# Kernel tuning notes

Measured on AMD Instinct MI355X. Metric: run time of the kernel, lower is better.

The kernel has to match this reference:

```python
import jax, jax.numpy as jnp
import numpy as np

N_NODES = 100000
N_EDGES = 1600000
VOCAB = 128
D = 30
N_CLASSES = 5


def setup_inputs() -> dict:
    key = jax.random.key(0)
    ks = jax.random.split(key, 8)
    x = jax.random.randint(ks[0], (N_NODES,), 0, VOCAB)
    edge_index = jax.random.randint(ks[1], (2, N_EDGES), 0, N_NODES)
    emb = jax.random.normal(ks[2], (VOCAB, D), dtype=jnp.float32)
    W1 = jax.random.normal(ks[3], (D, D), dtype=jnp.float32) * (1.0 / np.sqrt(D))
    W2 = jax.random.normal(ks[4], (D, D), dtype=jnp.float32) * (1.0 / np.sqrt(D))
    W3 = jax.random.normal(ks[5], (D, D), dtype=jnp.float32) * (1.0 / np.sqrt(D))
    Wout = jax.random.normal(ks[6], (N_CLASSES, D), dtype=jnp.float32) * (1.0 / np.sqrt(D))
    b1 = jnp.zeros((D,), jnp.float32)
    b2 = jnp.zeros((D,), jnp.float32)
    b3 = jnp.zeros((D,), jnp.float32)
    bout = jnp.zeros((N_CLASSES,), jnp.float32)
    return dict(x=x, edge_index=edge_index, emb=emb, W1=W1, b1=b1, W2=W2, b2=b2,
                W3=W3, b3=b3, Wout=Wout, bout=bout)


def _gnn_layer(h, row, col, W, b):
    # h: [N, D]; row/col: [E+N] (self loops appended)
    n = h.shape[0]
    deg = jax.ops.segment_sum(jnp.ones(row.shape, h.dtype), row, num_segments=n)  # [N]
    msg = h[row] / deg[row][:, None]                 # gather + normalize: [E+N, D]
    agg = jax.ops.segment_sum(msg, col, num_segments=n)  # scatter-add: [N, D]
    return jax.nn.relu(agg @ W.T + b)


def reference(x, edge_index, emb, W1, b1, W2, b2, W3, b3, Wout, bout):
    n = x.shape[0]
    loops = jnp.arange(n, dtype=edge_index.dtype)
    row = jnp.concatenate([edge_index[0], loops])  # add_self_loops
    col = jnp.concatenate([edge_index[1], loops])
    h = emb[x]  # [N, D]
    for W, b in ((W1, b1), (W2, b2), (W3, b3)):
        h = _gnn_layer(h, row, col, W, b)
    return h @ Wout.T + bout  # [N, 5]
```

## Files before the change

kernel.cpp:

```cpp
#include <hip/hip_runtime.h>
#include <hip/hip_fp16.h>

#define D 30
#define DP 32
#define NCLS 5
#define VOCAB 128
#define BS 256
#define BSS 512
#define BSHIFT 8
#define BNODES 256
#define NSBMAX 512
#define CAP 8192
#define NBLK_S 256
#define CHUNK 6272
#define LDSCAP 8192
#define NPB 64


__global__ void k_prep(int* __restrict__ gcur, int* __restrict__ rcur, int nsb,
                       const float* __restrict__ emb, float* __restrict__ embp,
                       __half* __restrict__ A0, __half* __restrict__ A1,
                       int2* __restrict__ xr, int n) {
    int i = blockIdx.x * blockDim.x + threadIdx.x;
    if (i < nsb) { gcur[i] = i * CAP; rcur[i] = i * CAP; }
    if (i < VOCAB * DP) {
        int v = i >> 5, c = i & (DP - 1);
        embp[i] = (c < D) ? emb[v * D + c] : 0.0f;
    }
    if (i < DP) {
        A0[(size_t)n * DP + i] = __float2half_rn(0.0f);
        A1[(size_t)n * DP + i] = __float2half_rn(0.0f);
    }
    if (i == 0) xr[n] = make_int2(0, 0);
}

__global__ void __launch_bounds__(BSS)
k_scatter3(const int* __restrict__ row, const int* __restrict__ col,
           int* __restrict__ gcur, int* __restrict__ rcur,
           int* __restrict__ ebuf, unsigned char* __restrict__ rbuf,
           int e, int nsb) {
    __shared__ int pay[CHUNK];
    __shared__ unsigned short bof[CHUNK];
    __shared__ int lhist[NSBMAX];
    __shared__ int lscan[NSBMAX];
    __shared__ int lcur[NSBMAX];
    __shared__ int gdst[NSBMAX];
    unsigned char* pay8 = (unsigned char*)pay;

    int phase = blockIdx.x >= NBLK_S;
    int blk = blockIdx.x - phase * NBLK_S;
    const int* key = phase ? row : col;
    int per = (e + NBLK_S - 1) / NBLK_S;
    int s = blk * per; if (s > e) s = e;
    int t = s + per; if (t > e) t = e;
    int m = t - s;
    int tid = threadIdx.x;

    lhist[tid] = 0;
    __syncthreads();
    for (int i = s + tid; i < t; i += BSS)
        atomicAdd(&lhist[key[i] >> BSHIFT], 1);
    __syncthreads();
    lscan[tid] = lhist[tid];
    __syncthreads();
    for (int st = 1; st < NSBMAX; st <<= 1) {
        int tv = (tid >= st) ? lscan[tid - st] : 0;
        __syncthreads();
        lscan[tid] += tv;
        __syncthreads();
    }
    lcur[tid] = lscan[tid] - lhist[tid];
    __syncthreads();
    if (phase == 0) {
        for (int i = s + tid; i < t; i += BSS) {
            int c = col[i], b = c >> BSHIFT;
            int p = atomicAdd(&lcur[b], 1);
            pay[p] = (row[i] << BSHIFT) | (c & (BNODES - 1));
            bof[p] = (unsigned short)b;
        }
    } else {
        for (int i = s + tid; i < t; i += BSS) {
            int r = row[i], b = r >> BSHIFT;
            int p = atomicAdd(&lcur[b], 1);
            pay8[p] = (unsigned char)(r & (BNODES - 1));
            bof[p] = (unsigned short)b;
        }
    }
    __syncthreads();
    int* cur = phase ? rcur : gcur;
    if (tid < nsb) {
        int h = lhist[tid];
        gdst[tid] = h ? atomicAdd(&cur[tid], h) : 0;
    }
    __syncthreads();
    if (phase == 0) {
        for (int p = tid; p < m; p += BSS) {
            int b = bof[p];
            ebuf[gdst[b] + (p - (lscan[b] - lhist[b]))] = pay[p];
        }
    } else {
        for (int p = tid; p < m; p += BSS) {
            int b = bof[p];
            rbuf[gdst[b] + (p - (lscan[b] - lhist[b]))] = pay8[p];
        }
    }
}

__global__ void __launch_bounds__(BS)
k_odbsort(int* __restrict__ ebuf, const unsigned char* __restrict__ rbuf,
          const int* __restrict__ gcur, const int* __restrict__ rcur,
          const int* __restrict__ x, float* __restrict__ rdeg, int2* __restrict__ xr,
          int* __restrict__ off, int* __restrict__ cnt, int n, int nsb) {
    __shared__ int ledge[LDSCAP];
    __shared__ int c256[BNODES];
    __shared__ int p256[BNODES];
    __shared__ int b256[BNODES];
    __shared__ int cur256[BNODES];
    int side = blockIdx.x >= nsb;
    int bkt = side ? blockIdx.x - nsb : blockIdx.x;
    int tid = threadIdx.x;
    int base = bkt * CAP;

    if (side == 0) {
        int rm = rcur[bkt] - base;
        c256[tid] = 0;
        __syncthreads();
        for (int k = tid; k < rm; k += BS)
            atomicAdd(&c256[rbuf[base + k]], 1);
        __syncthreads();
        int node = (bkt << BSHIFT) + tid;
        if (node < n) {
            float rd = 1.0f / (float)(c256[tid] + 1);
            rdeg[node] = rd;
            xr[node] = make_int2(x[node], __float_as_int(rd));
        }
    } else {
        int m = gcur[bkt] - base;
        if (m > LDSCAP) m = LDSCAP;
        for (int k = tid; k < m; k += BS) ledge[k] = ebuf[base + k];
        c256[tid] = 0;
        __syncthreads();
        for (int k = tid; k < m; k += BS)
            atomicAdd(&c256[ledge[k] & (BNODES - 1)], 1);
        __syncthreads();
        int pc = (c256[tid] + 7) & ~7;
        p256[tid] = pc;
        b256[tid] = pc;
        __syncthreads();
        for (int st = 1; st < BNODES; st <<= 1) {
            int tv = (tid >= st) ? b256[tid - st] : 0;
            __syncthreads();
            b256[tid] += tv;
            __syncthreads();
        }
        int mybase = base + b256[tid] - p256[tid];
        cur256[tid] = mybase;
        int node = (bkt << BSHIFT) + tid;
        if (node < n) {
            off[node] = mybase;
            cnt[node] = p256[tid];
        }
        __syncthreads();
        for (int k = tid; k < m; k += BS) {
            int v = ledge[k];
            int p = atomicAdd(&cur256[v & (BNODES - 1)], 1);
            ebuf[base + (p - base)] = v >> BSHIFT;
        }
        __syncthreads();
        int realend = cur256[tid];
        int padend = mybase + p256[tid];
        for (int p = realend; p < padend; ++p) ebuf[p] = n;
    }
}

__device__ __forceinline__ void acc8h(float4 raw, float* acc) {
    const __half2* h = (const __half2*)&raw;
#pragma unroll
    for (int u = 0; u < 4; ++u) {
        float2 f = __half22float2(h[u]);
        acc[2 * u] += f.x; acc[2 * u + 1] += f.y;
    }
}
__device__ __forceinline__ void fma4(float4 a, float4 w, float& d) {
    d = fmaf(a.x, w.x, d); d = fmaf(a.y, w.y, d);
    d = fmaf(a.z, w.z, d); d = fmaf(a.w, w.w, d);
}

__global__ void __launch_bounds__(BS)
k_agg_lin(const __half* __restrict__ Ain, const int2* __restrict__ xr,
          const float* __restrict__ embp,
          const int* __restrict__ off, const int* __restrict__ cnt,
          const int* __restrict__ esrc, const float* __restrict__ rdeg,
          const float* __restrict__ W, const float* __restrict__ bias,
          const float* __restrict__ Wout, const float* __restrict__ bout,
          __half* __restrict__ Aout, float* __restrict__ out,
          int n, int srcmode, int outmode) {
    __shared__ float aggS[NPB * DP];
    __shared__ float WsP[DP * DP];
    __shared__ float bsP[DP];
    __shared__ float WoP[NCLS * DP];
    __shared__ float boS[NCLS];
    const float4* Ain4  = (const float4*)Ain;
    const float4* embp4 = (const float4*)embp;
    int tid = threadIdx.x;
    int i0 = blockIdx.x * NPB;
    int j = tid >> 2;
    int q = tid & 3;
    int i = i0 + j;
    for (int p = tid; p < DP * DP; p += BS) {
        int rr = p >> 5, ccx = p & 31;
        WsP[p] = (rr < D && ccx < D) ? W[rr * D + ccx] : 0.0f;
    }
    if (tid < DP) bsP[tid] = (tid < D) ? bias[tid] : 0.0f;
    if (outmode == 1) {
        for (int p = tid; p < NCLS * DP; p += BS) {
            int rr = p >> 5, ccx = p & 31;
            WoP[p] = (ccx < D) ? Wout[rr * D + ccx] : 0.0f;
        }
        if (tid < NCLS) boS[tid] = bout[tid];
    }
    float acc[8];
#pragma unroll
    for (int u = 0; u < 8; ++u) acc[u] = 0.0f;
    if (i < n) {
        int base = off[i], c = cnt[i];
        if (srcmode == 0) {
            acc8h(Ain4[(size_t)i * 4 + q], acc);
            for (int k = 0; k < c; k += 8) {
                int4 ea = *(const int4*)(esrc + base + k);
                int4 eb = *(const int4*)(esrc + base + k + 4);
                float4 a0 = Ain4[(size_t)ea.x * 4 + q];
                float4 a1 = Ain4[(size_t)ea.y * 4 + q];
                float4 a2 = Ain4[(size_t)ea.z * 4 + q];
                float4 a3 = Ain4[(size_t)ea.w * 4 + q];
                float4 a4 = Ain4[(size_t)eb.x * 4 + q];
                float4 a5 = Ain4[(size_t)eb.y * 4 + q];
                float4 a6 = Ain4[(size_t)eb.z * 4 + q];
                float4 a7 = Ain4[(size_t)eb.w * 4 + q];
                acc8h(a0, acc); acc8h(a1, acc); acc8h(a2, acc); acc8h(a3, acc);
                acc8h(a4, acc); acc8h(a5, acc); acc8h(a6, acc); acc8h(a7, acc);
            }
        } else {
            int2 xi = xr[i];
            float ri = __int_as_float(xi.y);
            float4 e0 = embp4[(size_t)xi.x * 8 + 2 * q];
            float4 e1 = embp4[(size_t)xi.x * 8 + 2 * q + 1];
            acc[0] = e0.x * ri; acc[1] = e0.y * ri; acc[2] = e0.z * ri; acc[3] = e0.w * ri;
            acc[4] = e1.x * ri; acc[5] = e1.y * ri; acc[6] = e1.z * ri; acc[7] = e1.w * ri;
            for (int k = 0; k < c; k += 8) {
                int4 ea = *(const int4*)(esrc + base + k);
                int4 eb = *(const int4*)(esrc + base + k + 4);
                int2 xv[8];
                xv[0] = xr[ea.x]; xv[1] = xr[ea.y]; xv[2] = xr[ea.z]; xv[3] = xr[ea.w];
                xv[4] = xr[eb.x]; xv[5] = xr[eb.y]; xv[6] = xr[eb.z]; xv[7] = xr[eb.w];
#pragma unroll
                for (int u = 0; u < 8; ++u) {
                    float rr = __int_as_float(xv[u].y);
                    float4 f0 = embp4[(size_t)xv[u].x * 8 + 2 * q];
                    float4 f1 = embp4[(size_t)xv[u].x * 8 + 2 * q + 1];
                    acc[0] = fmaf(f0.x, rr, acc[0]); acc[1] = fmaf(f0.y, rr, acc[1]);
                    acc[2] = fmaf(f0.z, rr, acc[2]); acc[3] = fmaf(f0.w, rr, acc[3]);
                    acc[4] = fmaf(f1.x, rr, acc[4]); acc[5] = fmaf(f1.y, rr, acc[5]);
                    acc[6] = fmaf(f1.z, rr, acc[6]); acc[7] = fmaf(f1.w, rr, acc[7]);
                }
            }
        }
    }
    ((float4*)aggS)[j * 8 + 2 * q]     = make_float4(acc[0], acc[1], acc[2], acc[3]);
    ((float4*)aggS)[j * 8 + 2 * q + 1] = make_float4(acc[4], acc[5], acc[6], acc[7]);
    __syncthreads();

    {
        int cc = tid & 31;
        int jg = tid >> 5;
        const float4* wrow = (const float4*)&WsP[cc * DP];
        float4 w0 = wrow[0], w1 = wrow[1], w2 = wrow[2], w3 = wrow[3];
        float4 w4 = wrow[4], w5 = wrow[5], w6 = wrow[6], w7 = wrow[7];
        float bb = bsP[cc];
        if (outmode == 0) {
            for (int jj = jg; jj < NPB; jj += 8) {
                int nd = i0 + jj;
                if (nd >= n) break;
                const float4* ar = (const float4*)&aggS[jj * DP];
                float a = bb;
                fma4(ar[0], w0, a); fma4(ar[1], w1, a); fma4(ar[2], w2, a); fma4(ar[3], w3, a);
                fma4(ar[4], w4, a); fma4(ar[5], w5, a); fma4(ar[6], w6, a); fma4(ar[7], w7, a);
                a = fmaxf(a, 0.0f) * rdeg[nd];
                if (cc >= D) a = 0.0f;
                Aout[(size_t)nd * DP + cc] = __float2half_rn(a);
            }
        } else {
            float h3r[8];
#pragma unroll
            for (int u = 0; u < 8; ++u) {
                int jj = jg + 8 * u;
                const float4* ar = (const float4*)&aggS[jj * DP];
                float a = bb;
                fma4(ar[0], w0, a); fma4(ar[1], w1, a); fma4(ar[2], w2, a); fma4(ar[3], w3, a);
                fma4(ar[4], w4, a); fma4(ar[5], w5, a); fma4(ar[6], w6, a); fma4(ar[7], w7, a);
                h3r[u] = (cc < D) ? fmaxf(a, 0.0f) : 0.0f;
            }
            __syncthreads();
#pragma unroll
            for (int u = 0; u < 8; ++u)
                aggS[(jg + 8 * u) * DP + cc] = h3r[u];
            __syncthreads();
            for (int it = tid; it < NPB * NCLS; it += BS) {
                int jj = it / NCLS, cc2 = it - jj * NCLS;
                int nd = i0 + jj;
                if (nd >= n) continue;
                const float4* hr = (const float4*)&aggS[jj * DP];
                const float4* wr2 = (const float4*)&WoP[cc2 * DP];
                float a = boS[cc2];
#pragma unroll
                for (int u = 0; u < 8; ++u) fma4(hr[u], wr2[u], a);
                out[(size_t)nd * NCLS + cc2] = a;
            }
        }
    }
}


extern "C" void kernel_launch(void* const* d_in, const int* in_sizes, int n_in,
                              void* d_out, int out_size, void* d_ws, size_t ws_size,
                              hipStream_t stream) {
    const int*   x    = (const int*)d_in[0];
    const int*   ei   = (const int*)d_in[1];
    const float* emb  = (const float*)d_in[2];
    const float* W1   = (const float*)d_in[3];
    const float* b1   = (const float*)d_in[4];
    const float* W2   = (const float*)d_in[5];
    const float* b2   = (const float*)d_in[6];
    const float* W3   = (const float*)d_in[7];
    const float* b3   = (const float*)d_in[8];
    const float* Wout = (const float*)d_in[9];
    const float* bout = (const float*)d_in[10];
    float* out = (float*)d_out;

    const int N = in_sizes[0];
    const int E = in_sizes[1] / 2;
    const int* row = ei;
    const int* col = ei + E;
    const int nsb = (N + BNODES - 1) >> BSHIFT;

    __half* A0  = (__half*)d_ws;
    __half* A1  = A0 + (size_t)(N + 1) * DP;
    float* embp = (float*)(A1 + (size_t)(N + 1) * DP);
    float* rdeg = embp + VOCAB * DP;
    int2*  xr   = (int2*)(rdeg + N);
    int*   ebuf = (int*)(xr + N + 2);
    unsigned char* rbuf = (unsigned char*)(ebuf + (size_t)nsb * CAP);
    int*   off  = (int*)(rbuf + (((size_t)nsb * CAP + 3) & ~(size_t)3));
    int*   cnt  = off + N;
    int*   gcur = cnt + N;
    int*   rcur = gcur + nsb;

    dim3 blk(BS);

    k_prep<<<dim3((VOCAB * DP + BS - 1) / BS), blk, 0, stream>>>(
        gcur, rcur, nsb, emb, embp, A0, A1, xr, N);
    k_scatter3<<<dim3(2 * NBLK_S), dim3(BSS), 0, stream>>>(row, col, gcur, rcur,
                                                           ebuf, rbuf, E, nsb);
    k_odbsort<<<dim3(2 * nsb), blk, 0, stream>>>(ebuf, rbuf, gcur, rcur, x,
                                                 rdeg, xr, off, cnt, N, nsb);

    dim3 gAgg((N + NPB - 1) / NPB);
    k_agg_lin<<<gAgg, blk, 0, stream>>>(nullptr, xr, embp, off, cnt, ebuf, rdeg,
                                        W1, b1, Wout, bout, A1, out, N, 1, 0);
    k_agg_lin<<<gAgg, blk, 0, stream>>>(A1, xr, embp, off, cnt, ebuf, rdeg,
                                        W2, b2, Wout, bout, A0, out, N, 0, 0);
    k_agg_lin<<<gAgg, blk, 0, stream>>>(A0, xr, embp, off, cnt, ebuf, rdeg,
                                        W3, b3, Wout, bout, A1, out, N, 0, 1);
}
```

Baseline: 208.5 us.

## Materialize pre-scaled half embeddings and reuse generic gather path for layer one

Adds a k_embed kernel that writes emb[x]*rdeg as padded fp16 rows into A0, so layer one uses the same 16-byte half gather as the later layers. This replaces the per-edge xr lookup followed by two fp32 embedding float4 loads. It also drops the xr/embp buffers, adds a launch-bounds occupancy hint, and interleaves index loads with accumulation in the gather loop. The cost is an extra kernel launch, an extra pass writing N*32 halves, and fp16 rounding of the layer-one inputs.

Result: slower. 300.2 us (+43.9%).

```diff
diff --git a/kernel.cpp b/kernel.cpp
--- a/kernel.cpp
+++ b/kernel.cpp
@@ -4,7 +4,6 @@
 #define D 30
 #define DP 32
 #define NCLS 5
-#define VOCAB 128
 #define BS 256
 #define BSS 512
 #define BSHIFT 8
@@ -18,20 +17,13 @@
 
 
 __global__ void k_prep(int* __restrict__ gcur, int* __restrict__ rcur, int nsb,
-                       const float* __restrict__ emb, float* __restrict__ embp,
-                       __half* __restrict__ A0, __half* __restrict__ A1,
-                       int2* __restrict__ xr, int n) {
+                       __half* __restrict__ A0, __half* __restrict__ A1, int n) {
     int i = blockIdx.x * blockDim.x + threadIdx.x;
     if (i < nsb) { gcur[i] = i * CAP; rcur[i] = i * CAP; }
-    if (i < VOCAB * DP) {
-        int v = i >> 5, c = i & (DP - 1);
-        embp[i] = (c < D) ? emb[v * D + c] : 0.0f;
-    }
     if (i < DP) {
         A0[(size_t)n * DP + i] = __float2half_rn(0.0f);
         A1[(size_t)n * DP + i] = __float2half_rn(0.0f);
     }
-    if (i == 0) xr[n] = make_int2(0, 0);
 }
 
 __global__ void __launch_bounds__(BSS)
@@ -109,7 +101,7 @@
 __global__ void __launch_bounds__(BS)
 k_odbsort(int* __restrict__ ebuf, const unsigned char* __restrict__ rbuf,
           const int* __restrict__ gcur, const int* __restrict__ rcur,
-          const int* __restrict__ x, float* __restrict__ rdeg, int2* __restrict__ xr,
+          float* __restrict__ rdeg,
           int* __restrict__ off, int* __restrict__ cnt, int n, int nsb) {
     __shared__ int ledge[LDSCAP];
     __shared__ int c256[BNODES];
@@ -129,11 +121,8 @@
             atomicAdd(&c256[rbuf[base + k]], 1);
         __syncthreads();
         int node = (bkt << BSHIFT) + tid;
-        if (node < n) {
-            float rd = 1.0f / (float)(c256[tid] + 1);
-            rdeg[node] = rd;
-            xr[node] = make_int2(x[node], __float_as_int(rd));
-        }
+        if (node < n)
+            rdeg[node] = 1.0f / (float)(c256[tid] + 1);
     } else {
         int m = gcur[bkt] - base;
         if (m > LDSCAP) m = LDSCAP;
@@ -164,7 +153,7 @@
         for (int k = tid; k < m; k += BS) {
             int v = ledge[k];
             int p = atomicAdd(&cur256[v & (BNODES - 1)], 1);
-            ebuf[base + (p - base)] = v >> BSHIFT;
+            ebuf[p] = v >> BSHIFT;
         }
         __syncthreads();
         int realend = cur256[tid];
@@ -173,6 +162,17 @@
     }
 }
 
+
+__global__ void k_embed(const int* __restrict__ x, const float* __restrict__ emb,
+                        const float* __restrict__ rdeg, __half* __restrict__ A, int n) {
+    int tid = blockIdx.x * blockDim.x + threadIdx.x;
+    if (tid >= n * DP) return;
+    int i = tid >> 5, c = tid & (DP - 1);
+    float v = 0.0f;
+    if (c < D) v = emb[x[i] * D + c] * rdeg[i];
+    A[tid] = __float2half_rn(v);
+}
+
 __device__ __forceinline__ void acc8h(float4 raw, float* acc) {
     const __half2* h = (const __half2*)&raw;
 #pragma unroll
@@ -186,22 +186,20 @@
     d = fmaf(a.z, w.z, d); d = fmaf(a.w, w.w, d);
 }
 
-__global__ void __launch_bounds__(BS)
-k_agg_lin(const __half* __restrict__ Ain, const int2* __restrict__ xr,
-          const float* __restrict__ embp,
+__global__ void __launch_bounds__(BS, 8)
+k_agg_lin(const __half* __restrict__ Ain,
           const int* __restrict__ off, const int* __restrict__ cnt,
           const int* __restrict__ esrc, const float* __restrict__ rdeg,
           const float* __restrict__ W, const float* __restrict__ bias,
           const float* __restrict__ Wout, const float* __restrict__ bout,
           __half* __restrict__ Aout, float* __restrict__ out,
-          int n, int srcmode, int outmode) {
+          int n, int outmode) {
     __shared__ float aggS[NPB * DP];
     __shared__ float WsP[DP * DP];
     __shared__ float bsP[DP];
     __shared__ float WoP[NCLS * DP];
     __shared__ float boS[NCLS];
-    const float4* Ain4  = (const float4*)Ain;
-    const float4* embp4 = (const float4*)embp;
+    const float4* Ain4 = (const float4*)Ain;
     int tid = threadIdx.x;
     int i0 = blockIdx.x * NPB;
     int j = tid >> 2;
@@ -224,46 +222,20 @@
     for (int u = 0; u < 8; ++u) acc[u] = 0.0f;
     if (i < n) {
         int base = off[i], c = cnt[i];
-        if (srcmode == 0) {
-            acc8h(Ain4[(size_t)i * 4 + q], acc);
-            for (int k = 0; k < c; k += 8) {
-                int4 ea = *(const int4*)(esrc + base + k);
-                int4 eb = *(const int4*)(esrc + base + k + 4);
-                float4 a0 = Ain4[(size_t)ea.x * 4 + q];
-                float4 a1 = Ain4[(size_t)ea.y * 4 + q];
-                float4 a2 = Ain4[(size_t)ea.z * 4 + q];
-                float4 a3 = Ain4[(size_t)ea.w * 4 + q];
-                float4 a4 = Ain4[(size_t)eb.x * 4 + q];
-                float4 a5 = Ain4[(size_t)eb.y * 4 + q];
-                float4 a6 = Ain4[(size_t)eb.z * 4 + q];
-                float4 a7 = Ain4[(size_t)eb.w * 4 + q];
-                acc8h(a0, acc); acc8h(a1, acc); acc8h(a2, acc); acc8h(a3, acc);
-                acc8h(a4, acc); acc8h(a5, acc); acc8h(a6, acc); acc8h(a7, acc);
-            }
-        } else {
-            int2 xi = xr[i];
-            float ri = __int_as_float(xi.y);
-            float4 e0 = embp4[(size_t)xi.x * 8 + 2 * q];
-            float4 e1 = embp4[(size_t)xi.x * 8 + 2 * q + 1];
-            acc[0] = e0.x * ri; acc[1] = e0.y * ri; acc[2] = e0.z * ri; acc[3] = e0.w * ri;
-            acc[4] = e1.x * ri; acc[5] = e1.y * ri; acc[6] = e1.z * ri; acc[7] = e1.w * ri;
-            for (int k = 0; k < c; k += 8) {
-                int4 ea = *(const int4*)(esrc + base + k);
-                int4 eb = *(const int4*)(esrc + base + k + 4);
-                int2 xv[8];
-                xv[0] = xr[ea.x]; xv[1] = xr[ea.y]; xv[2] = xr[ea.z]; xv[3] = xr[ea.w];
-                xv[4] = xr[eb.x]; xv[5] = xr[eb.y]; xv[6] = xr[eb.z]; xv[7] = xr[eb.w];
-#pragma unroll
-                for (int u = 0; u < 8; ++u) {
-                    float rr = __int_as_float(xv[u].y);
-                    float4 f0 = embp4[(size_t)xv[u].x * 8 + 2 * q];
-                    float4 f1 = embp4[(size_t)xv[u].x * 8 + 2 * q + 1];
-                    acc[0] = fmaf(f0.x, rr, acc[0]); acc[1] = fmaf(f0.y, rr, acc[1]);
-                    acc[2] = fmaf(f0.z, rr, acc[2]); acc[3] = fmaf(f0.w, rr, acc[3]);
-                    acc[4] = fmaf(f1.x, rr, acc[4]); acc[5] = fmaf(f1.y, rr, acc[5]);
-                    acc[6] = fmaf(f1.z, rr, acc[6]); acc[7] = fmaf(f1.w, rr, acc[7]);
-                }
-            }
+        acc8h(Ain4[(size_t)i * 4 + q], acc);
+        for (int k = 0; k < c; k += 8) {
+            int4 ea = *(const int4*)(esrc + base + k);
+            float4 a0 = Ain4[(size_t)ea.x * 4 + q];
+            float4 a1 = Ain4[(size_t)ea.y * 4 + q];
+            float4 a2 = Ain4[(size_t)ea.z * 4 + q];
+            float4 a3 = Ain4[(size_t)ea.w * 4 + q];
+            int4 eb = *(const int4*)(esrc + base + k + 4);
+            acc8h(a0, acc); acc8h(a1, acc); acc8h(a2, acc); acc8h(a3, acc);
+            float4 a4 = Ain4[(size_t)eb.x * 4 + q];
+            float4 a5 = Ain4[(size_t)eb.y * 4 + q];
+            float4 a6 = Ain4[(size_t)eb.z * 4 + q];
+            float4 a7 = Ain4[(size_t)eb.w * 4 + q];
+            acc8h(a4, acc); acc8h(a5, acc); acc8h(a6, acc); acc8h(a7, acc);
         }
     }
     ((float4*)aggS)[j * 8 + 2 * q]     = make_float4(acc[0], acc[1], acc[2], acc[3]);
@@ -274,8 +246,6 @@
         int cc = tid & 31;
         int jg = tid >> 5;
         const float4* wrow = (const float4*)&WsP[cc * DP];
-        float4 w0 = wrow[0], w1 = wrow[1], w2 = wrow[2], w3 = wrow[3];
-        float4 w4 = wrow[4], w5 = wrow[5], w6 = wrow[6], w7 = wrow[7];
         float bb = bsP[cc];
         if (outmode == 0) {
             for (int jj = jg; jj < NPB; jj += 8) {
@@ -283,8 +253,8 @@
                 if (nd >= n) break;
                 const float4* ar = (const float4*)&aggS[jj * DP];
                 float a = bb;
-                fma4(ar[0], w0, a); fma4(ar[1], w1, a); fma4(ar[2], w2, a); fma4(ar[3], w3, a);
-                fma4(ar[4], w4, a); fma4(ar[5], w5, a); fma4(ar[6], w6, a); fma4(ar[7], w7, a);
+#pragma unroll
+                for (int u = 0; u < 8; ++u) fma4(ar[u], wrow[u], a);
                 a = fmaxf(a, 0.0f) * rdeg[nd];
                 if (cc >= D) a = 0.0f;
                 Aout[(size_t)nd * DP + cc] = __float2half_rn(a);
@@ -296,8 +266,8 @@
                 int jj = jg + 8 * u;
                 const float4* ar = (const float4*)&aggS[jj * DP];
                 float a = bb;
-                fma4(ar[0], w0, a); fma4(ar[1], w1, a); fma4(ar[2], w2, a); fma4(ar[3], w3, a);
-                fma4(ar[4], w4, a); fma4(ar[5], w5, a); fma4(ar[6], w6, a); fma4(ar[7], w7, a);
+#pragma unroll
+                for (int v = 0; v < 8; ++v) fma4(ar[v], wrow[v], a);
                 h3r[u] = (cc < D) ? fmaxf(a, 0.0f) : 0.0f;
             }
             __syncthreads();
@@ -345,10 +315,8 @@
 
     __half* A0  = (__half*)d_ws;
     __half* A1  = A0 + (size_t)(N + 1) * DP;
-    float* embp = (float*)(A1 + (size_t)(N + 1) * DP);
-    float* rdeg = embp + VOCAB * DP;
-    int2*  xr   = (int2*)(rdeg + N);
-    int*   ebuf = (int*)(xr + N + 2);
+    float* rdeg = (float*)(A1 + (size_t)(N + 1) * DP);
+    int*   ebuf = (int*)(rdeg + N);
     unsigned char* rbuf = (unsigned char*)(ebuf + (size_t)nsb * CAP);
     int*   off  = (int*)(rbuf + (((size_t)nsb * CAP + 3) & ~(size_t)3));
     int*   cnt  = off + N;
@@ -357,18 +325,18 @@
 
     dim3 blk(BS);
 
-    k_prep<<<dim3((VOCAB * DP + BS - 1) / BS), blk, 0, stream>>>(
-        gcur, rcur, nsb, emb, embp, A0, A1, xr, N);
+    k_prep<<<dim3(2), blk, 0, stream>>>(gcur, rcur, nsb, A0, A1, N);
     k_scatter3<<<dim3(2 * NBLK_S), dim3(BSS), 0, stream>>>(row, col, gcur, rcur,
                                                            ebuf, rbuf, E, nsb);
-    k_odbsort<<<dim3(2 * nsb), blk, 0, stream>>>(ebuf, rbuf, gcur, rcur, x,
-                                                 rdeg, xr, off, cnt, N, nsb);
+    k_odbsort<<<dim3(2 * nsb), blk, 0, stream>>>(ebuf, rbuf, gcur, rcur,
+                                                 rdeg, off, cnt, N, nsb);
+    k_embed<<<dim3(((size_t)N * DP + BS - 1) / BS), blk, 0, stream>>>(x, emb, rdeg, A0, N);
 
     dim3 gAgg((N + NPB - 1) / NPB);
-    k_agg_lin<<<gAgg, blk, 0, stream>>>(nullptr, xr, embp, off, cnt, ebuf, rdeg,
-                                        W1, b1, Wout, bout, A1, out, N, 1, 0);
-    k_agg_lin<<<gAgg, blk, 0, stream>>>(A1, xr, embp, off, cnt, ebuf, rdeg,
-                                        W2, b2, Wout, bout, A0, out, N, 0, 0);
-    k_agg_lin<<<gAgg, blk, 0, stream>>>(A0, xr, embp, off, cnt, ebuf, rdeg,
-                                        W3, b3, Wout, bout, A1, out, N, 0, 1);
-}
+    k_agg_lin<<<gAgg, blk, 0, stream>>>(A0, off, cnt, ebuf, rdeg,
+                                        W1, b1, Wout, bout, A1, out, N, 0);
+    k_agg_lin<<<gAgg, blk, 0, stream>>>(A1, off, cnt, ebuf, rdeg,
+                                        W2, b2, Wout, bout, A0, out, N, 0);
+    k_agg_lin<<<gAgg, blk, 0, stream>>>(A0, off, cnt, ebuf, rdeg,
+                                        W3, b3, Wout, bout, A1, out, N, 1);
+}
```
